# Optimization experiments

Measured on AMD Instinct MI355X. Metric: run time of the kernel, lower is better.

The kernel has to match this reference:

```python
import jax, jax.numpy as jnp
import numpy as np

EPS = 1e-5
DIM = 128
SCALE = DIM ** (-0.5)


def setup_inputs() -> dict:
    key = jax.random.key(0)
    k1, k2, k3 = jax.random.split(key, 3)
    B, N, D = 2, 128 * 128, DIM
    Q = N // 4
    x = jax.random.normal(k1, (B, N, D), dtype=jnp.float32)
    gamma = jnp.ones((D,), dtype=jnp.float32)
    beta = jnp.zeros((D,), dtype=jnp.float32)
    queries = jax.random.normal(k2, (Q, D), dtype=jnp.float32)
    W = jax.random.normal(k3, (2 * D, D), dtype=jnp.float32) * (1.0 / np.sqrt(D))
    return {"x": x, "gamma": gamma, "beta": beta, "queries": queries, "W": W}


def reference(x, gamma, beta, queries, W):
    # LayerNorm over last dim (eps matches torch default 1e-5)
    mu = jnp.mean(x, axis=-1, keepdims=True)
    var = jnp.mean(jnp.square(x - mu), axis=-1, keepdims=True)
    xn = (x - mu) * jax.lax.rsqrt(var + EPS) * gamma + beta  # [B, N, D]
    # learned-query cross attention: sim = Q @ xn^T * scale -> softmax -> @ xn
    sim = jnp.einsum('qd,bnd->bqn', queries, xn) * SCALE     # [B, Q, N]
    attn = jax.nn.softmax(sim, axis=-1)
    out = jnp.einsum('bqn,bnd->bqd', attn, xn)               # [B, Q, D]
    # trailing linear: dim -> 2*dim, no bias
    return jnp.einsum('bqd,ed->bqe', out, W)                 # [B, Q, 2D]
```

## Files before the change

### kernel.cpp

```cpp
#include <hip/hip_runtime.h>
#include <stdint.h>

#define Nn 16384
#define Dd 128
#define Qq 4096
#define Ee 256
#define KV 64

typedef __bf16 bf16x8 __attribute__((ext_vector_type(8)));
typedef float floatx16 __attribute__((ext_vector_type(16)));
typedef unsigned uintx2 __attribute__((ext_vector_type(2)));

__device__ __forceinline__ float fexp2(float x) {
#if __has_builtin(__builtin_amdgcn_exp2f)
  return __builtin_amdgcn_exp2f(x);
#else
  return exp2f(x);
#endif
}
__device__ __forceinline__ unsigned pk_bf(float lo, float hi) {
  return __builtin_amdgcn_perm(__float_as_uint(hi) + 0x8000u,
                               __float_as_uint(lo) + 0x8000u, 0x07060302u);
}
__device__ __forceinline__ void stage16(const void* g, void* lds_uniform) {
  __builtin_amdgcn_global_load_lds(
      (const __attribute__((address_space(1))) unsigned int*)g,
      (__attribute__((address_space(3))) unsigned int*)lds_uniform, 16, 0, 0);
}
__device__ __forceinline__ void plswap(unsigned a, unsigned b, int hi,
                                       unsigned& r0, unsigned& r1) {
#if __has_builtin(__builtin_amdgcn_permlane32_swap)
  uintx2 r = __builtin_amdgcn_permlane32_swap(a, b, false, false);
  r0 = r[0];
  r1 = r[1];
  (void)hi;
#else
  unsigned ax = __shfl_xor(a, 32);
  unsigned bx = __shfl_xor(b, 32);
  r0 = hi ? bx : a;
  r1 = hi ? b : ax;
#endif
}

__global__ __launch_bounds__(256) void k_lnt(
    const float* __restrict__ x, const float* __restrict__ gamma,
    const float* __restrict__ beta, const float* __restrict__ queries,
    const float* __restrict__ W, unsigned* __restrict__ xn,
    unsigned short* __restrict__ xnT, unsigned short* __restrict__ qb,
    unsigned short* __restrict__ wb) {
  __shared__ __align__(16) uint2 lds2[64 * 32];
  const int tid = threadIdx.x;
  const int bid = blockIdx.x;
  const int b = bid >> 8, n0 = (bid & 255) * 64;
  const int r = tid >> 2, qd = tid & 3;

  const float4* xp = (const float4*)(x + ((size_t)(b * Nn + n0 + r)) * Dd + qd * 32);
  float4 v[8];
  float s = 0.f, s2 = 0.f;
#pragma unroll
  for (int i = 0; i < 8; ++i) {
    v[i] = xp[i];
    s += (v[i].x + v[i].y) + (v[i].z + v[i].w);
    s2 += (v[i].x * v[i].x + v[i].y * v[i].y) + (v[i].z * v[i].z + v[i].w * v[i].w);
  }
  s += __shfl_xor(s, 1); s2 += __shfl_xor(s2, 1);
  s += __shfl_xor(s, 2); s2 += __shfl_xor(s2, 2);
  float mu = s * (1.0f / 128.0f);
  float var = s2 * (1.0f / 128.0f) - mu * mu;
  float rs = rsqrtf(var + 1e-5f);

  const float4* gp = (const float4*)(gamma + qd * 32);
  const float4* bp = (const float4*)(beta + qd * 32);
  unsigned pk[16];
#pragma unroll
  for (int i = 0; i < 8; ++i) {
    float4 g = gp[i], bt = bp[i];
    pk[2 * i] = pk_bf((v[i].x - mu) * rs * g.x + bt.x, (v[i].y - mu) * rs * g.y + bt.y);
    pk[2 * i + 1] = pk_bf((v[i].z - mu) * rs * g.z + bt.z, (v[i].w - mu) * rs * g.w + bt.w);
  }
  unsigned* xrow = xn + ((size_t)(b * Nn + n0 + r)) * 64;
#pragma unroll
  for (int j = 0; j < 4; ++j)
    *(uint4*)(xrow + (((qd * 4 + j) ^ (r & 7)) * 4)) =
        make_uint4(pk[4 * j], pk[4 * j + 1], pk[4 * j + 2], pk[4 * j + 3]);
  const int rk = r & 31;
#pragma unroll
  for (int kk = 0; kk < 8; ++kk)
    lds2[r * 32 + ((qd * 8 + kk) ^ rk)] = make_uint2(pk[2 * kk], pk[2 * kk + 1]);
  __syncthreads();
  const int dq = tid >> 3, nc = tid & 7;
  uint2 U[8];
#pragma unroll
  for (int j = 0; j < 8; ++j) {
    int rr = nc * 8 + j;
    U[j] = lds2[rr * 32 + (dq ^ (rr & 31))];
  }
#pragma unroll
  for (int e = 0; e < 4; ++e) {
    int d = dq * 4 + e;
    unsigned a0 = (e & 2) ? U[0].y : U[0].x, a1 = (e & 2) ? U[1].y : U[1].x;
    unsigned a2 = (e & 2) ? U[2].y : U[2].x, a3 = (e & 2) ? U[3].y : U[3].x;
    unsigned a4 = (e & 2) ? U[4].y : U[4].x, a5 = (e & 2) ? U[5].y : U[5].x;
    unsigned a6 = (e & 2) ? U[6].y : U[6].x, a7 = (e & 2) ? U[7].y : U[7].x;
    unsigned sel = (e & 1) ? 0x07060302u : 0x05040100u;
    uint4 o;
    o.x = __builtin_amdgcn_perm(a1, a0, sel);
    o.y = __builtin_amdgcn_perm(a3, a2, sel);
    o.z = __builtin_amdgcn_perm(a5, a4, sel);
    o.w = __builtin_amdgcn_perm(a7, a6, sel);
    *(uint4*)(xnT + ((size_t)(b * Dd + d)) * Nn + n0 + (nc ^ (d & 7)) * 8) = o;
  }
  const float QSC = 0.08838834764831845f * 1.4426950408889634f;
  const int total4 = (Qq * Dd + Ee * Dd) / 4;
  for (int u = bid * 256 + tid; u < total4; u += 512 * 256) {
    if (u < Qq * Dd / 4) {
      float4 v4 = ((const float4*)queries)[u];
      ((uint2*)qb)[u] = make_uint2(pk_bf(v4.x * QSC, v4.y * QSC),
                                   pk_bf(v4.z * QSC, v4.w * QSC));
    } else {
      float4 v4 = ((const float4*)W)[u - Qq * Dd / 4];
      ((uint2*)wb)[u - Qq * Dd / 4] =
          make_uint2(pk_bf(v4.x, v4.y), pk_bf(v4.z, v4.w));
    }
  }
}

template <int NS, int NWAVE>
__global__ __launch_bounds__(NWAVE * 64, NWAVE / 2) void k_attn(
    const unsigned short* __restrict__ xn,
    const unsigned short* __restrict__ xnT,
    const unsigned short* __restrict__ qb,
    float* __restrict__ o_part,
    float* __restrict__ l_part) {
  constexpr int NCH = Nn / NS;
  constexpr int NIT = NCH / KV;
  constexpr int QT = Qq / (32 * NWAVE);
  constexpr int CPW = 16 / NWAVE;
  __shared__ __align__(16) char lds[2][32768];

  const int bid = blockIdx.x;
  const int split = bid % NS;
  const int qt = (bid / NS) % QT;
  const int b = bid / (NS * QT);
  const int tid = threadIdx.x;
  const int wave = tid >> 6, lane = tid & 63;
  const int col = lane & 31, half = lane >> 5;
  const int ck = col & 7;
  const int qwbase = qt * (32 * NWAVE) + wave * 32;

  bf16x8 qf[8];
#pragma unroll
  for (int s = 0; s < 8; ++s)
    qf[s] = *(const bf16x8*)(qb + (size_t)(qwbase + col) * Dd + s * 16 + half * 8);

  const floatx16 fz = {0.f,0.f,0.f,0.f,0.f,0.f,0.f,0.f,0.f,0.f,0.f,0.f,0.f,0.f,0.f,0.f};
  floatx16 O[4];
#pragma unroll
  for (int d = 0; d < 4; ++d) O[d] = fz;
  float lsum = 0.f;

  const char* gx = (const char*)xn + (size_t)b * Nn * 256;
  const char* gxt = (const char*)xnT + (size_t)b * Dd * Nn * 2;
  const int tbase = split * NCH / KV;

  auto stageTile = [&](int t, char* dst) {
    const char* xsrc = gx + (size_t)(tbase + t) * (KV * 256);
#pragma unroll
    for (int p = 0; p < CPW; ++p) {
      int m = wave * CPW + p;
      stage16(xsrc + m * 1024 + lane * 16, dst + m * 1024);
    }
#pragma unroll
    for (int p = 0; p < CPW; ++p) {
      int m = wave * CPW + p;
      const char* g = gxt + (size_t)(m * 8 + (lane >> 3)) * (Nn * 2) +
                      (size_t)(tbase + t) * (KV * 2) + (lane & 7) * 16;
      stage16(g, dst + 16384 + m * 1024);
    }
  };

  stageTile(0, &lds[0][0]);
  if (NIT > 1) stageTile(1, &lds[1][0]);

  int cur = 0;
#pragma unroll 1
  for (int i = 0; i < NIT; ++i) {
    if (i + 1 < NIT) {
      asm volatile("s_waitcnt vmcnt(8)" ::: "memory");
    } else {
      asm volatile("s_waitcnt vmcnt(0)" ::: "memory");
    }
    __builtin_amdgcn_s_barrier();
    __builtin_amdgcn_sched_barrier(0);

    const char* lx = &lds[0][0] + (cur << 15);
    const char* lxt = lx + 16384;

    floatx16 S[2];
    S[0] = fz; S[1] = fz;
    __builtin_amdgcn_s_setprio(1);
#pragma unroll
    for (int s = 0; s < 8; ++s)
#pragma unroll
      for (int mt = 0; mt < 2; ++mt) {
        bf16x8 ax = *(const bf16x8*)(lx + (32 * mt + col) * 256 +
                                     (((2 * s + half) ^ ck) * 16));
        S[mt] = __builtin_amdgcn_mfma_f32_32x32x16_bf16(ax, qf[s], S[mt], 0, 0, 0);
      }
    __builtin_amdgcn_s_setprio(0);

    unsigned P[2][4][2];
#pragma unroll
    for (int mt = 0; mt < 2; ++mt)
#pragma unroll
      for (int t = 0; t < 4; ++t) {
        float p0 = fexp2(S[mt][4 * t]);
        float p1 = fexp2(S[mt][4 * t + 1]);
        float p2 = fexp2(S[mt][4 * t + 2]);
        float p3 = fexp2(S[mt][4 * t + 3]);
        lsum += (p0 + p1) + (p2 + p3);
        P[mt][t][0] = pk_bf(p0, p1);
        P[mt][t][1] = pk_bf(p2, p3);
      }

    __builtin_amdgcn_s_setprio(1);
#pragma unroll
    for (int s2 = 0; s2 < 4; ++s2) {
      const int mt = s2 >> 1, ge = 2 * (s2 & 1), go = ge + 1;
      unsigned w0, w1, w2, w3;
      plswap(P[mt][ge][0], P[mt][go][0], half, w0, w2);
      plswap(P[mt][ge][1], P[mt][go][1], half, w1, w3);
      union { uint4 u; bf16x8 v; } ap;
      ap.u = make_uint4(w0, w1, w2, w3);
#pragma unroll
      for (int dn = 0; dn < 4; ++dn) {
        bf16x8 bx = *(const bf16x8*)(lxt + (32 * dn + col) * 128 +
                                     (((2 * s2 + half) ^ ck) * 16));
        O[dn] = __builtin_amdgcn_mfma_f32_32x32x16_bf16(ap.v, bx, O[dn], 0, 0, 0);
      }
    }
    __builtin_amdgcn_s_setprio(0);

    __builtin_amdgcn_s_barrier();
    if (i + 2 < NIT) stageTile(i + 2, &lds[0][0] + (cur << 15));
    cur ^= 1;
  }

  float lt = lsum + __shfl_xor(lsum, 32);
  if (half == 0)
    l_part[(size_t)(b * NS + split) * Qq + qwbase + col] = lt;
  float* op = o_part + ((size_t)(b * NS + split) * Qq + qwbase) * Dd;
#pragma unroll
  for (int dn = 0; dn < 4; ++dn)
#pragma unroll
    for (int r = 0; r < 16; ++r) {
      int q = (r & 3) + 8 * (r >> 2) + 4 * half;
      op[(size_t)q * Dd + dn * 32 + col] = O[dn][r];
    }
}

template <int NS>
__global__ __launch_bounds__(256) void k_comb(
    const float* __restrict__ o_part, const float* __restrict__ l_part,
    const unsigned short* __restrict__ wb, float* __restrict__ out) {
  __shared__ __align__(16) char lds_a[32 * 256];
  __shared__ float lds_linv[32];
  const int bid = blockIdx.x;
  const int b = bid >> 7, qc = bid & 127;
  const int qbase = qc * 32;
  const int tid = threadIdx.x;
  const int wave = tid >> 6, lane = tid & 63;
  const int col = lane & 31, half = lane >> 5;
  const int ck = col & 7;

  if (tid < 32) {
    float l = 0.f;
#pragma unroll
    for (int s = 0; s < NS; ++s)
      l += l_part[(size_t)(b * NS + s) * Qq + qbase + tid];
    lds_linv[tid] = 1.0f / l;
  }
  __syncthreads();

#pragma unroll
  for (int i = 0; i < 4; ++i) {
    int idx = i * 256 + tid;
    int q = idx >> 5, d4 = idx & 31;
    float4 acc = make_float4(0.f, 0.f, 0.f, 0.f);
#pragma unroll
    for (int s = 0; s < NS; ++s) {
      float4 v = *(const float4*)(o_part + ((size_t)(b * NS + s) * Qq + qbase + q) * Dd + d4 * 4);
      acc.x += v.x; acc.y += v.y; acc.z += v.z; acc.w += v.w;
    }
    float li = lds_linv[q];
    int w = d4 >> 1;
    int pos = (w & 8) | ((w ^ (q & 7)) & 7);
    *(uint2*)(lds_a + q * 256 + pos * 16 + (d4 & 1) * 8) =
        make_uint2(pk_bf(acc.x * li, acc.y * li), pk_bf(acc.z * li, acc.w * li));
  }
  __syncthreads();

  bf16x8 af[8];
#pragma unroll
  for (int s = 0; s < 8; ++s) {
    int u = 2 * s + half;
    int pos = (u & 8) | ((u ^ ck) & 7);
    af[s] = *(const bf16x8*)(lds_a + col * 256 + pos * 16);
  }

  const floatx16 fz = {0.f,0.f,0.f,0.f,0.f,0.f,0.f,0.f,0.f,0.f,0.f,0.f,0.f,0.f,0.f,0.f};
#pragma unroll
  for (int et = 0; et < 2; ++et) {
    floatx16 C = fz;
    int e_row = wave * 64 + et * 32 + col;
#pragma unroll
    for (int s = 0; s < 8; ++s) {
      bf16x8 bw = *(const bf16x8*)(wb + (size_t)e_row * Dd + s * 16 + half * 8);
      C = __builtin_amdgcn_mfma_f32_32x32x16_bf16(af[s], bw, C, 0, 0, 0);
    }
#pragma unroll
    for (int r = 0; r < 16; ++r) {
      int q = qbase + (r & 3) + 8 * (r >> 2) + 4 * half;
      out[((size_t)b * Qq + q) * Ee + wave * 64 + et * 32 + col] = C[r];
    }
  }
}

extern "C" void kernel_launch(void* const* d_in, const int* in_sizes, int n_in,
                              void* d_out, int out_size, void* d_ws, size_t ws_size,
                              hipStream_t stream) {
  const float* x = (const float*)d_in[0];
  const float* gamma = (const float*)d_in[1];
  const float* beta = (const float*)d_in[2];
  const float* queries = (const float*)d_in[3];
  const float* W = (const float*)d_in[4];
  float* out = (float*)d_out;

  char* w = (char*)d_ws;
  unsigned short* xn = (unsigned short*)(w);
  unsigned short* xnT = (unsigned short*)(w + 8388608);
  unsigned short* qb = (unsigned short*)(w + 16777216);
  unsigned short* wb = (unsigned short*)(w + 17825792);
  float* o_part = (float*)(w + 17891328);
  float* l_part = (float*)(w + 51445760);

  k_lnt<<<dim3(512), dim3(256), 0, stream>>>(x, gamma, beta, queries, W,
                                             (unsigned*)xn, xnT, qb, wb);
  k_attn<8, 4><<<dim3(512), dim3(256), 0, stream>>>(xn, xnT, qb, o_part, l_part);
  k_comb<8><<<dim3(256), dim3(256), 0, stream>>>(o_part, l_part, wb, out);
}
```

Baseline: 158.8 us.

## Software-pipeline attention loop to overlap softmax exp with next tile's MFMAs

Restructures the attention main loop so that each iteration runs the QK^T MFMAs for tile i and the PV MFMAs for tile i-1 back to back, then does the exp/pack for tile i. This lets the exp work overlap matrix-core work instead of sitting between the two MFMA phases. It needs separate X and X^T LDS buffers, with a triple-buffered X^T because PV now lags by one tile. The cost is more LDS per block (80KB instead of 64KB), plus a prologue and epilogue. The launch-bounds occupancy hint is also fixed at 2.

```diff
diff --git a/kernel.cpp b/kernel.cpp
--- a/kernel.cpp
+++ b/kernel.cpp
@@ -126,7 +126,7 @@
 }
 
 template <int NS, int NWAVE>
-__global__ __launch_bounds__(NWAVE * 64, NWAVE / 2) void k_attn(
+__global__ __launch_bounds__(NWAVE * 64, 2) void k_attn(
     const unsigned short* __restrict__ xn,
     const unsigned short* __restrict__ xnT,
     const unsigned short* __restrict__ qb,
@@ -136,7 +136,8 @@
   constexpr int NIT = NCH / KV;
   constexpr int QT = Qq / (32 * NWAVE);
   constexpr int CPW = 16 / NWAVE;
-  __shared__ __align__(16) char lds[2][32768];
+  __shared__ __align__(16) char lds_x[2][16384];
+  __shared__ __align__(16) char lds_xt[3][16384];
 
   const int bid = blockIdx.x;
   const int split = bid % NS;
@@ -163,42 +164,24 @@
   const char* gxt = (const char*)xnT + (size_t)b * Dd * Nn * 2;
   const int tbase = split * NCH / KV;
 
-  auto stageTile = [&](int t, char* dst) {
+  auto stgX = [&](int t, int buf) {
     const char* xsrc = gx + (size_t)(tbase + t) * (KV * 256);
 #pragma unroll
     for (int p = 0; p < CPW; ++p) {
       int m = wave * CPW + p;
-      stage16(xsrc + m * 1024 + lane * 16, dst + m * 1024);
-    }
+      stage16(xsrc + m * 1024 + lane * 16, &lds_x[buf][0] + m * 1024);
+    }
+  };
+  auto stgXT = [&](int t, int buf) {
 #pragma unroll
     for (int p = 0; p < CPW; ++p) {
       int m = wave * CPW + p;
       const char* g = gxt + (size_t)(m * 8 + (lane >> 3)) * (Nn * 2) +
                       (size_t)(tbase + t) * (KV * 2) + (lane & 7) * 16;
-      stage16(g, dst + 16384 + m * 1024);
-    }
-  };
-
-  stageTile(0, &lds[0][0]);
-  if (NIT > 1) stageTile(1, &lds[1][0]);
-
-  int cur = 0;
-#pragma unroll 1
-  for (int i = 0; i < NIT; ++i) {
-    if (i + 1 < NIT) {
-      asm volatile("s_waitcnt vmcnt(8)" ::: "memory");
-    } else {
-      asm volatile("s_waitcnt vmcnt(0)" ::: "memory");
-    }
-    __builtin_amdgcn_s_barrier();
-    __builtin_amdgcn_sched_barrier(0);
-
-    const char* lx = &lds[0][0] + (cur << 15);
-    const char* lxt = lx + 16384;
-
-    floatx16 S[2];
-    S[0] = fz; S[1] = fz;
-    __builtin_amdgcn_s_setprio(1);
+      stage16(g, &lds_xt[buf][0] + m * 1024);
+    }
+  };
+  auto sphase = [&](const char* lx, floatx16* S) {
 #pragma unroll
     for (int s = 0; s < 8; ++s)
 #pragma unroll
@@ -207,9 +190,8 @@
                                      (((2 * s + half) ^ ck) * 16));
         S[mt] = __builtin_amdgcn_mfma_f32_32x32x16_bf16(ax, qf[s], S[mt], 0, 0, 0);
       }
-    __builtin_amdgcn_s_setprio(0);
-
-    unsigned P[2][4][2];
+  };
+  auto expphase = [&](const floatx16* S, unsigned P[2][4][2]) {
 #pragma unroll
     for (int mt = 0; mt < 2; ++mt)
 #pragma unroll
@@ -222,8 +204,8 @@
         P[mt][t][0] = pk_bf(p0, p1);
         P[mt][t][1] = pk_bf(p2, p3);
       }
-
-    __builtin_amdgcn_s_setprio(1);
+  };
+  auto pvphase = [&](const char* lxt, unsigned P[2][4][2]) {
 #pragma unroll
     for (int s2 = 0; s2 < 4; ++s2) {
       const int mt = s2 >> 1, ge = 2 * (s2 & 1), go = ge + 1;
@@ -239,12 +221,53 @@
         O[dn] = __builtin_amdgcn_mfma_f32_32x32x16_bf16(ap.v, bx, O[dn], 0, 0, 0);
       }
     }
+  };
+
+  stgX(0, 0); stgXT(0, 0);
+  stgX(1, 1); stgXT(1, 1);
+  asm volatile("s_waitcnt vmcnt(8)" ::: "memory");
+  __builtin_amdgcn_s_barrier();
+  __builtin_amdgcn_sched_barrier(0);
+
+  unsigned P[2][4][2];
+  {
+    floatx16 S[2]; S[0] = fz; S[1] = fz;
+    __builtin_amdgcn_s_setprio(1);
+    sphase(&lds_x[0][0], S);
     __builtin_amdgcn_s_setprio(0);
-
+    expphase(S, P);
+  }
+  asm volatile("" ::: "memory");
+  __builtin_amdgcn_s_barrier();
+  if (NIT > 2) { stgX(2, 0); stgXT(2, 2); }
+
+  int xtc = 0;
+#pragma unroll 1
+  for (int i = 1; i < NIT; ++i) {
+    if (i + 1 < NIT) {
+      asm volatile("s_waitcnt vmcnt(8)" ::: "memory");
+    } else {
+      asm volatile("s_waitcnt vmcnt(0)" ::: "memory");
+    }
     __builtin_amdgcn_s_barrier();
-    if (i + 2 < NIT) stageTile(i + 2, &lds[0][0] + (cur << 15));
-    cur ^= 1;
-  }
+    __builtin_amdgcn_sched_barrier(0);
+
+    const char* lx = &lds_x[i & 1][0];
+    const char* lxt = &lds_xt[xtc][0];
+
+    floatx16 S[2]; S[0] = fz; S[1] = fz;
+    __builtin_amdgcn_s_setprio(1);
+    sphase(lx, S);
+    pvphase(lxt, P);
+    __builtin_amdgcn_s_setprio(0);
+    expphase(S, P);
+
+    asm volatile("" ::: "memory");
+    __builtin_amdgcn_s_barrier();
+    if (i + 2 < NIT) { stgX(i + 2, i & 1); stgXT(i + 2, xtc); }
+    xtc = (xtc == 2) ? 0 : xtc + 1;
+  }
+  pvphase(&lds_xt[xtc][0], P);
 
   float lt = lsum + __shfl_xor(lsum, 32);
   if (half == 0)
```

Result: no change. 158.7 us (-0.0%).
